# Performance work log

Hardware: AMD Instinct MI355X
Metric: run time of the kernel (lower is better)

The kernel has to match this reference:

```python
import jax, jax.numpy as jnp
import numpy as np

TWO_PI = 2.0 * np.pi
D_IN, N, P, C, BATCH = 784, 1024, 128, 10, 256
T, BETA, K_COUP, A_ANC = 0.5, 2.0, 1.0, 0.08
OMEGA_ANC = TWO_PI * 200.0
N_STEPS = 16  # fixed-grid RK4 steps over [0, T]


def setup_inputs() -> dict:
    key = jax.random.key(0)
    k0, k1, k2, k3 = jax.random.split(key, 4)
    x = jax.random.normal(k0, (BATCH, D_IN), dtype=jnp.float32)
    W_enc = jax.random.normal(k1, (N, D_IN), dtype=jnp.float32) * (1.0 / np.sqrt(D_IN))
    b_enc = jnp.zeros((N,), dtype=jnp.float32)
    xi = jax.random.uniform(k2, (P, N), dtype=jnp.float32) * TWO_PI  # memory patterns
    W_out = jax.random.normal(k3, (C, 2 * N), dtype=jnp.float32) * (1.0 / np.sqrt(2 * N))
    b_out = jnp.zeros((C,), dtype=jnp.float32)
    return {"x": x, "W_enc": W_enc, "b_enc": b_enc, "xi": xi, "W_out": W_out, "b_out": b_out}


def _dphi(t, phi, xi):
    # phi: (B, N), xi: (P, N) -> diff: (B, P, N)
    diff = phi[:, None, :] - xi[None, :, :]
    m = jnp.cos(diff).sum(-1)                               # (B, P) overlaps
    w = jax.nn.softmax(BETA * m / N, axis=-1)               # (B, P)
    coupling = jnp.einsum('bp,bpn->bn', w, jnp.sin(diff))   # (B, N)
    return K_COUP * coupling + A_ANC * jnp.sin(OMEGA_ANC * t - phi)


def reference(x, W_enc, b_enc, xi, W_out, b_out):
    # Encoder: phi0 in (0, 2pi)
    phi0 = TWO_PI * jax.nn.sigmoid(x @ W_enc.T + b_enc)
    dt = T / N_STEPS

    def step(phi, t):
        k1 = _dphi(t, phi, xi)
        k2 = _dphi(t + 0.5 * dt, phi + 0.5 * dt * k1, xi)
        k3 = _dphi(t + 0.5 * dt, phi + 0.5 * dt * k2, xi)
        k4 = _dphi(t + dt, phi + dt * k3, xi)
        return phi + (dt / 6.0) * (k1 + 2.0 * k2 + 2.0 * k3 + k4), None

    ts = jnp.arange(N_STEPS, dtype=jnp.float32) * dt
    phi_T, _ = jax.lax.scan(step, phi0, ts)
    # Readout on [cos, sin] features
    feats = jnp.concatenate([jnp.cos(phi_T), jnp.sin(phi_T)], axis=-1)
    return feats @ W_out.T + b_out
```

## Files before the change

kernel.cpp:

```cpp
#include <hip/hip_runtime.h>
#include <math.h>


typedef __attribute__((ext_vector_type(4))) float f32x4;
typedef __attribute__((ext_vector_type(4))) int   i32x4;
typedef __attribute__((ext_vector_type(8))) short bf16x8;
typedef __attribute__((ext_vector_type(2))) unsigned short u16x2;

struct TCons { float s[64]; float c[64]; };

__device__ __forceinline__ unsigned short f2bf(float f) {
  unsigned u = __builtin_bit_cast(unsigned, f);
  return (unsigned short)((u + 0x7FFFu + ((u >> 16) & 1u)) >> 16);
}
__device__ __forceinline__ int pk4i8(const float* v) {
  int a = __float2int_rn(v[0]*127.0f) & 255;
  int b = __float2int_rn(v[1]*127.0f) & 255;
  int c = __float2int_rn(v[2]*127.0f) & 255;
  int d = __float2int_rn(v[3]*127.0f);
  return a | (b << 8) | (c << 16) | (d << 24);
}

#define A1_OFF    0
#define MBUF_OFF  8192
#define W_OFF     10304
#define ZP_OFF    10560
#define XST_OFF   10576
#define T2L_OFF   13904
#define RED_OFF   13904
#define LDS_BYTES 161360

__global__
__attribute__((amdgpu_flat_work_group_size(1024, 1024), amdgpu_waves_per_eu(4, 4)))
void phasenn_kernel(
    const float* __restrict__ x, const float* __restrict__ W_enc,
    const float* __restrict__ b_enc, const float* __restrict__ xi,
    const float* __restrict__ W_out, const float* __restrict__ b_out,
    float* __restrict__ dout, char* __restrict__ wsb, TCons tc)
{
  __shared__ __align__(16) char smem[LDS_BYTES];

  const int tid  = threadIdx.x;
  const int bk   = blockIdx.x;
  const int w    = tid >> 6;
  const int lane = tid & 63;
  const int q    = lane >> 4;
  const int b16  = lane & 15;
  const int row2 = b16 & 1;
  const int j4   = b16 >> 2;
  const int rp   = (b16 >> 1) & 1;

  char* T1g = wsb;
  char* T2g = wsb + (256 << 10);

  if (tid < 4) *(unsigned*)(smem + ZP_OFF + tid*4) = 0;

  {
    const int row = tid >> 7, dg = tid & 127;
    if (row < 2 && dg < 100) {
      bf16x8 fr = {0,0,0,0,0,0,0,0};
      if (dg < 98) {
        f32x4 v0 = *(const f32x4*)(x + (bk*2 + row)*784 + dg*8);
        f32x4 v1 = *(const f32x4*)(x + (bk*2 + row)*784 + dg*8 + 4);
        #pragma unroll
        for (int i = 0; i < 8; ++i) fr[i] = (short)f2bf(i < 4 ? v0[i] : v1[i-4]);
      }
      *(bf16x8*)(smem + XST_OFF + row*1664 + (((dg ^ row) & 127) << 4)) = fr;
    }
  }

  if (w < 8) {
    const int p = w*16 + b16;
    for (int F = 0; F < 16; ++F) {
      const int n0 = F*64 + q*16;
      f32x4 v0 = *(const f32x4*)(xi + p*1024 + n0);
      f32x4 v1 = *(const f32x4*)(xi + p*1024 + n0 + 4);
      f32x4 v2 = *(const f32x4*)(xi + p*1024 + n0 + 8);
      f32x4 v3 = *(const f32x4*)(xi + p*1024 + n0 + 12);
      float cv[16], sv[16];
      #pragma unroll
      for (int i = 0; i < 16; ++i) {
        float xv = (i < 4) ? v0[i] : (i < 8) ? v1[i-4] : (i < 12) ? v2[i-8] : v3[i-12];
        sv[i] = __sinf(xv); cv[i] = __cosf(xv);
      }
      i32x4 C = { pk4i8(cv), pk4i8(cv+4), pk4i8(cv+8), pk4i8(cv+12) };
      i32x4 S = { pk4i8(sv), pk4i8(sv+4), pk4i8(sv+8), pk4i8(sv+12) };
      char* dst = T1g + (size_t)(w*16 + F)*2048 + lane*16;
      *(i32x4*)(dst) = C; *(i32x4*)(dst + 1024) = S;
    }
  } else {
    const int w2 = w - 8;
    for (int f = 0; f < 16; ++f) {
      const int ct = w2*8 + (f >> 1), P2 = f & 1;
      const int n = ct*16 + b16;
      float cv[16], sv[16];
      #pragma unroll
      for (int i = 0; i < 16; ++i) {
        float xv = xi[(P2*64 + q*16 + i)*1024 + n];
        sv[i] = __sinf(xv); cv[i] = __cosf(xv);
      }
      i32x4 C = { pk4i8(cv), pk4i8(cv+4), pk4i8(cv+8), pk4i8(cv+12) };
      i32x4 S = { pk4i8(sv), pk4i8(sv+4), pk4i8(sv+8), pk4i8(sv+12) };
      char* dst = (ct < 36)
          ? (smem + T2L_OFF + (size_t)(ct*2 + P2)*2048 + lane*16)
          : (T2g + (size_t)(ct*2 + P2)*2048 + lane*16);
      *(i32x4*)(dst) = C; *(i32x4*)(dst + 1024) = S;
    }
  }
  __syncthreads();

  float p0[2], ka[2], pwv[2];
  {
    f32x4 pac[4] = {{0,0,0,0},{0,0,0,0},{0,0,0,0},{0,0,0,0}};
    for (int kt = 0; kt < 25; ++kt) {
      const char* baddr =
          smem + XST_OFF + row2*1664 + ((((kt*4 + q) ^ row2) & 127) << 4);
      bf16x8 bfr = *(const bf16x8*)baddr;
      const int d = kt*32 + q*8;
      #pragma unroll
      for (int j = 0; j < 4; ++j) {
        bf16x8 afr = {0,0,0,0,0,0,0,0};
        if (d < 784) {
          const int n = (w*4 + j)*16 + b16;
          f32x4 v0 = *(const f32x4*)(W_enc + n*784 + d);
          f32x4 v1 = *(const f32x4*)(W_enc + n*784 + d + 4);
          #pragma unroll
          for (int i = 0; i < 8; ++i) afr[i] = (short)f2bf(i < 4 ? v0[i] : v1[i-4]);
        }
        pac[j] = __builtin_amdgcn_mfma_f32_16x16x32_bf16(afr, bfr, pac[j], 0, 0, 0);
      }
    }
    f32x4 pc = (j4==0) ? pac[0] : (j4==1) ? pac[1] : (j4==2) ? pac[2] : pac[3];
    float vA = rp ? pc[2] : pc[0];
    float vB = rp ? pc[3] : pc[1];
    const int n0 = (w*4 + j4)*16 + q*4 + rp*2;
    float ph0 = 6.283185307179586f / (1.0f + __expf(-(vA + b_enc[n0])));
    float ph1 = 6.283185307179586f / (1.0f + __expf(-(vB + b_enc[n0 + 1])));
    p0[0] = ph0; pwv[0] = ph0; ka[0] = 0.0f;
    p0[1] = ph1; pwv[1] = ph1; ka[1] = 0.0f;
  }

  const float dtf = 0.03125f, half = 0.015625f;
  const float sixth = (float)(0.03125/6.0);
  const float mscale = (float)(2.0 / (1024.0 * 16129.0));
  const float kscale = (float)(1.0 / 16129.0);

  for (int e = 0; e < 64; ++e) {
    float csv[2], snv[2];
    {
      #pragma unroll
      for (int r = 0; r < 2; ++r) {
        snv[r] = __sinf(pwv[r]);
        csv[r] = __cosf(pwv[r]);
      }
      int c0 = __float2int_rn(csv[0]*127.0f) & 255;
      int c1 = __float2int_rn(csv[1]*127.0f) & 255;
      int s0 = __float2int_rn(snv[0]*127.0f) & 255;
      int s1 = __float2int_rn(snv[1]*127.0f) & 255;
      const int n0 = (w*4 + j4)*16 + q*4 + rp*2;
      char* base = smem + A1_OFF + row2*2048 + n0;
      *(unsigned short*)(base)        = (unsigned short)(c0 | (c1 << 8));
      *(unsigned short*)(base + 1024) = (unsigned short)(s0 | (s1 << 8));
    }
    __syncthreads();

    {
      const int pt = w & 7, kh = w >> 3;
      i32x4 accC = {0,0,0,0}, accS = {0,0,0,0};
      const char* t1b = T1g + (size_t)(pt*16 + kh*8)*2048 + lane*16;
      const char* a1b = smem + A1_OFF + row2*2048;
      #pragma unroll
      for (int i2 = 0; i2 < 8; ++i2) {
        const int F = kh*8 + i2;
        i32x4 ca = *(const i32x4*)(t1b + (size_t)i2*2048);
        i32x4 sa = *(const i32x4*)(t1b + (size_t)i2*2048 + 1024);
        i32x4 bc = *(const i32x4*)(a1b + F*64 + q*16);
        i32x4 bs = *(const i32x4*)(a1b + 1024 + F*64 + q*16);
        accC = __builtin_amdgcn_mfma_i32_16x16x64_i8(ca, bc, accC, 0, 0, 0);
        accS = __builtin_amdgcn_mfma_i32_16x16x64_i8(sa, bs, accS, 0, 0, 0);
      }
      if (b16 < 2) {
        i32x4 acc = accC + accS;
        *(i32x4*)(smem + MBUF_OFF + kh*1056 + b16*528 + ((pt*16 + q*4) << 2)) = acc;
      }
    }
    __syncthreads();

    if (w < 2) {
      const char* mb = smem + MBUF_OFF + w*528 + lane*8;
      int a0 = *(const int*)(mb),        a1 = *(const int*)(mb + 4);
      int b0 = *(const int*)(mb + 1056), b1 = *(const int*)(mb + 1056 + 4);
      float e0 = __expf((float)(a0 + b0) * mscale);
      float e1 = __expf((float)(a1 + b1) * mscale);
      float s = e0 + e1;
      #pragma unroll
      for (int off = 1; off < 64; off <<= 1) s += __shfl_xor(s, off, 64);
      const float inv = 127.0f / s;
      int w0 = __float2int_rn(e0 * inv);
      int w1 = __float2int_rn(e1 * inv);
      *(unsigned short*)(smem + W_OFF + w*128 + lane*2) =
          (unsigned short)((w0 & 255) | (w1 << 8));
    }
    __syncthreads();

    {
      const float swt = tc.s[e], cwt = tc.c[e];
      const int st = e & 3;
      i32x4 wf0 = *(const i32x4*)(smem + W_OFF + row2*128 + q*16);
      i32x4 wf1 = *(const i32x4*)(smem + W_OFF + row2*128 + 64 + q*16);
      i32x4 aC[4] = {{0,0,0,0},{0,0,0,0},{0,0,0,0},{0,0,0,0}};
      i32x4 aS[4] = {{0,0,0,0},{0,0,0,0},{0,0,0,0},{0,0,0,0}};
      if (w < 9) {
        const char* t2b = smem + T2L_OFF + (size_t)(w*8)*2048 + lane*16;
        #pragma unroll
        for (int c = 0; c < 4; ++c)
          #pragma unroll
          for (int P2 = 0; P2 < 2; ++P2) {
            i32x4 ct_ = *(const i32x4*)(t2b + (size_t)(c*2 + P2)*2048);
            i32x4 st_ = *(const i32x4*)(t2b + (size_t)(c*2 + P2)*2048 + 1024);
            i32x4 wf = P2 ? wf1 : wf0;
            aC[c] = __builtin_amdgcn_mfma_i32_16x16x64_i8(ct_, wf, aC[c], 0, 0, 0);
            aS[c] = __builtin_amdgcn_mfma_i32_16x16x64_i8(st_, wf, aS[c], 0, 0, 0);
          }
      } else {
        const char* t2b = T2g + (size_t)(w*8)*2048 + lane*16;
        #pragma unroll
        for (int c = 0; c < 4; ++c)
          #pragma unroll
          for (int P2 = 0; P2 < 2; ++P2) {
            i32x4 ct_ = *(const i32x4*)(t2b + (size_t)(c*2 + P2)*2048);
            i32x4 st_ = *(const i32x4*)(t2b + (size_t)(c*2 + P2)*2048 + 1024);
            i32x4 wf = P2 ? wf1 : wf0;
            aC[c] = __builtin_amdgcn_mfma_i32_16x16x64_i8(ct_, wf, aC[c], 0, 0, 0);
            aS[c] = __builtin_amdgcn_mfma_i32_16x16x64_i8(st_, wf, aS[c], 0, 0, 0);
          }
      }
      i32x4 c4 = (j4==0) ? aC[0] : (j4==1) ? aC[1] : (j4==2) ? aC[2] : aC[3];
      i32x4 s4 = (j4==0) ? aS[0] : (j4==1) ? aS[1] : (j4==2) ? aS[2] : aS[3];
      float vC[2], vS[2];
      vC[0] = (float)(rp ? c4[2] : c4[0]);  vC[1] = (float)(rp ? c4[3] : c4[1]);
      vS[0] = (float)(rp ? s4[2] : s4[0]);  vS[1] = (float)(rp ? s4[3] : s4[1]);
      #pragma unroll
      for (int r = 0; r < 2; ++r) {
        float s_ = snv[r];
        float c_ = csv[r];
        float kv = (s_*vC[r] - c_*vS[r]) * kscale
                 + 0.08f*(swt*c_ - cwt*s_);
        if (st == 0)      { ka[r]  = kv;           pwv[r] = p0[r] + kv*half; }
        else if (st == 1) { ka[r] += 2.0f*kv;      pwv[r] = p0[r] + kv*half; }
        else if (st == 2) { ka[r] += 2.0f*kv;      pwv[r] = p0[r] + kv*dtf;  }
        else { ka[r] += kv; p0[r] += ka[r]*sixth; pwv[r] = p0[r]; }
      }
    }
  }

  __syncthreads();
  {
    u16x2 cp, sp;
    #pragma unroll
    for (int r = 0; r < 2; ++r) {
      float ph = p0[r];
      cp[r] = f2bf(__cosf(ph)); sp[r] = f2bf(__sinf(ph));
    }
    const int cj = (w*4 + j4)*2 + (q >> 1);
    char* base = smem + A1_OFF + row2*4096 + ((q & 1) << 3) + rp*4;
    *(u16x2*)(base + ((cj ^ row2) << 4))        = cp;
    *(u16x2*)(base + ((cj ^ row2) << 4) + 2048) = sp;
  }
  __syncthreads();
  {
    f32x4 acc = {0.f, 0.f, 0.f, 0.f};
    #pragma unroll
    for (int i2 = 0; i2 < 4; ++i2) {
      const int kt = w*4 + i2;
      const int k = kt*32 + q*8;
      bf16x8 afr = {0,0,0,0,0,0,0,0};
      if (b16 < 10) {
        f32x4 v0 = *(const f32x4*)(W_out + b16*2048 + k);
        f32x4 v1 = *(const f32x4*)(W_out + b16*2048 + k + 4);
        #pragma unroll
        for (int i = 0; i < 8; ++i) afr[i] = (short)f2bf(i < 4 ? v0[i] : v1[i-4]);
      }
      const char* baddr = (b16 < 2)
          ? (smem + A1_OFF + b16*4096 + ((((kt*4 + q) ^ b16) & 255) << 4))
          : (smem + ZP_OFF);
      bf16x8 bfr = *(const bf16x8*)baddr;
      acc = __builtin_amdgcn_mfma_f32_16x16x32_bf16(afr, bfr, acc, 0, 0, 0);
    }
    *(f32x4*)(smem + RED_OFF + ((w*64 + lane) << 4)) = acc;
  }
  __syncthreads();
  if (tid < 64) {
    f32x4 s = {0.f, 0.f, 0.f, 0.f};
    #pragma unroll
    for (int w2 = 0; w2 < 16; ++w2)
      s += *(const f32x4*)(smem + RED_OFF + ((w2*64 + tid) << 4));
    const int b = tid & 15, q2 = tid >> 4;
    if (b < 2) {
      #pragma unroll
      for (int r = 0; r < 4; ++r) {
        const int cl = q2*4 + r;
        if (cl < 10)
          dout[(bk*2 + b)*10 + cl] = s[r] + b_out[cl];
      }
    }
  }
}

extern "C" void kernel_launch(void* const* d_in, const int* in_sizes, int n_in,
                              void* d_out, int out_size, void* d_ws, size_t ws_size,
                              hipStream_t stream) {
  (void)in_sizes; (void)n_in; (void)ws_size; (void)out_size;
  const float* x     = (const float*)d_in[0];
  const float* W_enc = (const float*)d_in[1];
  const float* b_enc = (const float*)d_in[2];
  const float* xi    = (const float*)d_in[3];
  const float* W_out = (const float*)d_in[4];
  const float* b_out = (const float*)d_in[5];
  float* out = (float*)d_out;
  char* wsb = (char*)d_ws;

  TCons tc;
  const double OME = 2.0 * 3.14159265358979323846 * 200.0;
  const double dtd = 0.03125;
  const double co[4] = {0.0, 0.5, 0.5, 1.0};
  for (int e = 0; e < 64; ++e) {
    double t = ((double)(e >> 2) + co[e & 3]) * dtd;
    tc.s[e] = (float)sin(OME * t);
    tc.c[e] = (float)cos(OME * t);
  }

  phasenn_kernel<<<dim3(128), dim3(1024), 0, stream>>>(
      x, W_enc, b_enc, xi, W_out, b_out, out, wsb, tc);
}
```

Measured before the change: 410.3 us.

## Process one sample per block and double grid to fill all CUs

Each block now handles a single batch row instead of two, and the launch grid doubles to 256 blocks. Per-block MFMA work stays about the same because the batch dimension was only padding in 16-wide tiles, so this spreads the work across twice as many compute units. The trade-off is redundant per-block setup and weight-table loads, plus more global/L2 traffic for the shared pattern tables.

Measured after the change: 400.2 us. 1.03x faster.

```diff
diff --git a/kernel.cpp b/kernel.cpp
--- a/kernel.cpp
+++ b/kernel.cpp
@@ -5,7 +5,6 @@
 typedef __attribute__((ext_vector_type(4))) float f32x4;
 typedef __attribute__((ext_vector_type(4))) int   i32x4;
 typedef __attribute__((ext_vector_type(8))) short bf16x8;
-typedef __attribute__((ext_vector_type(2))) unsigned short u16x2;
 
 struct TCons { float s[64]; float c[64]; };
 
@@ -22,13 +21,13 @@
 }
 
 #define A1_OFF    0
-#define MBUF_OFF  8192
-#define W_OFF     10304
-#define ZP_OFF    10560
-#define XST_OFF   10576
-#define T2L_OFF   13904
-#define RED_OFF   13904
-#define LDS_BYTES 161360
+#define MBUF_OFF  4096
+#define W_OFF     5152
+#define ZP_OFF    5408
+#define XST_OFF   5424
+#define T2L_OFF   7104
+#define RED_OFF   7104
+#define LDS_BYTES 154560
 
 __global__
 __attribute__((amdgpu_flat_work_group_size(1024, 1024), amdgpu_waves_per_eu(4, 4)))
@@ -46,27 +45,25 @@
   const int lane = tid & 63;
   const int q    = lane >> 4;
   const int b16  = lane & 15;
-  const int row2 = b16 & 1;
   const int j4   = b16 >> 2;
-  const int rp   = (b16 >> 1) & 1;
+  const int r4   = b16 & 3;
+  const int nph  = (w*4 + j4)*16 + q*4 + r4;
 
   char* T1g = wsb;
   char* T2g = wsb + (256 << 10);
 
   if (tid < 4) *(unsigned*)(smem + ZP_OFF + tid*4) = 0;
 
-  {
-    const int row = tid >> 7, dg = tid & 127;
-    if (row < 2 && dg < 100) {
-      bf16x8 fr = {0,0,0,0,0,0,0,0};
-      if (dg < 98) {
-        f32x4 v0 = *(const f32x4*)(x + (bk*2 + row)*784 + dg*8);
-        f32x4 v1 = *(const f32x4*)(x + (bk*2 + row)*784 + dg*8 + 4);
-        #pragma unroll
-        for (int i = 0; i < 8; ++i) fr[i] = (short)f2bf(i < 4 ? v0[i] : v1[i-4]);
-      }
-      *(bf16x8*)(smem + XST_OFF + row*1664 + (((dg ^ row) & 127) << 4)) = fr;
-    }
+  if (tid < 100) {
+    const int dg = tid;
+    bf16x8 fr = {0,0,0,0,0,0,0,0};
+    if (dg < 98) {
+      f32x4 v0 = *(const f32x4*)(x + (size_t)bk*784 + dg*8);
+      f32x4 v1 = *(const f32x4*)(x + (size_t)bk*784 + dg*8 + 4);
+      #pragma unroll
+      for (int i = 0; i < 8; ++i) fr[i] = (short)f2bf(i < 4 ? v0[i] : v1[i-4]);
+    }
+    *(bf16x8*)(smem + XST_OFF + (dg << 4)) = fr;
   }
 
   if (w < 8) {
@@ -109,13 +106,11 @@
   }
   __syncthreads();
 
-  float p0[2], ka[2], pwv[2];
+  float p0, ka, pwv;
   {
     f32x4 pac[4] = {{0,0,0,0},{0,0,0,0},{0,0,0,0},{0,0,0,0}};
     for (int kt = 0; kt < 25; ++kt) {
-      const char* baddr =
-          smem + XST_OFF + row2*1664 + ((((kt*4 + q) ^ row2) & 127) << 4);
-      bf16x8 bfr = *(const bf16x8*)baddr;
+      bf16x8 bfr = *(const bf16x8*)(smem + XST_OFF + ((kt*4 + q) << 4));
       const int d = kt*32 + q*8;
       #pragma unroll
       for (int j = 0; j < 4; ++j) {
@@ -131,13 +126,9 @@
       }
     }
     f32x4 pc = (j4==0) ? pac[0] : (j4==1) ? pac[1] : (j4==2) ? pac[2] : pac[3];
-    float vA = rp ? pc[2] : pc[0];
-    float vB = rp ? pc[3] : pc[1];
-    const int n0 = (w*4 + j4)*16 + q*4 + rp*2;
-    float ph0 = 6.283185307179586f / (1.0f + __expf(-(vA + b_enc[n0])));
-    float ph1 = 6.283185307179586f / (1.0f + __expf(-(vB + b_enc[n0 + 1])));
-    p0[0] = ph0; pwv[0] = ph0; ka[0] = 0.0f;
-    p0[1] = ph1; pwv[1] = ph1; ka[1] = 0.0f;
+    float vA = (r4==0) ? pc[0] : (r4==1) ? pc[1] : (r4==2) ? pc[2] : pc[3];
+    float ph = 6.283185307179586f / (1.0f + __expf(-(vA + b_enc[nph])));
+    p0 = ph; pwv = ph; ka = 0.0f;
   }
 
   const float dtf = 0.03125f, half = 0.015625f;
@@ -145,22 +136,15 @@
   const float mscale = (float)(2.0 / (1024.0 * 16129.0));
   const float kscale = (float)(1.0 / 16129.0);
 
+  char* a1wr = smem + A1_OFF + nph;
+
   for (int e = 0; e < 64; ++e) {
-    float csv[2], snv[2];
+    float csv, snv;
     {
-      #pragma unroll
-      for (int r = 0; r < 2; ++r) {
-        snv[r] = __sinf(pwv[r]);
-        csv[r] = __cosf(pwv[r]);
-      }
-      int c0 = __float2int_rn(csv[0]*127.0f) & 255;
-      int c1 = __float2int_rn(csv[1]*127.0f) & 255;
-      int s0 = __float2int_rn(snv[0]*127.0f) & 255;
-      int s1 = __float2int_rn(snv[1]*127.0f) & 255;
-      const int n0 = (w*4 + j4)*16 + q*4 + rp*2;
-      char* base = smem + A1_OFF + row2*2048 + n0;
-      *(unsigned short*)(base)        = (unsigned short)(c0 | (c1 << 8));
-      *(unsigned short*)(base + 1024) = (unsigned short)(s0 | (s1 << 8));
+      snv = __sinf(pwv);
+      csv = __cosf(pwv);
+      *(char*)(a1wr)        = (char)(__float2int_rn(csv*127.0f));
+      *(char*)(a1wr + 1024) = (char)(__float2int_rn(snv*127.0f));
     }
     __syncthreads();
 
@@ -168,28 +152,27 @@
       const int pt = w & 7, kh = w >> 3;
       i32x4 accC = {0,0,0,0}, accS = {0,0,0,0};
       const char* t1b = T1g + (size_t)(pt*16 + kh*8)*2048 + lane*16;
-      const char* a1b = smem + A1_OFF + row2*2048;
+      const char* a1b = smem + A1_OFF + kh*512 + q*16;
       #pragma unroll
       for (int i2 = 0; i2 < 8; ++i2) {
-        const int F = kh*8 + i2;
         i32x4 ca = *(const i32x4*)(t1b + (size_t)i2*2048);
         i32x4 sa = *(const i32x4*)(t1b + (size_t)i2*2048 + 1024);
-        i32x4 bc = *(const i32x4*)(a1b + F*64 + q*16);
-        i32x4 bs = *(const i32x4*)(a1b + 1024 + F*64 + q*16);
+        i32x4 bc = *(const i32x4*)(a1b + i2*64);
+        i32x4 bs = *(const i32x4*)(a1b + i2*64 + 1024);
         accC = __builtin_amdgcn_mfma_i32_16x16x64_i8(ca, bc, accC, 0, 0, 0);
         accS = __builtin_amdgcn_mfma_i32_16x16x64_i8(sa, bs, accS, 0, 0, 0);
       }
-      if (b16 < 2) {
+      if (b16 == 0) {
         i32x4 acc = accC + accS;
-        *(i32x4*)(smem + MBUF_OFF + kh*1056 + b16*528 + ((pt*16 + q*4) << 2)) = acc;
+        *(i32x4*)(smem + MBUF_OFF + kh*528 + ((pt*16 + q*4) << 2)) = acc;
       }
     }
     __syncthreads();
 
-    if (w < 2) {
-      const char* mb = smem + MBUF_OFF + w*528 + lane*8;
-      int a0 = *(const int*)(mb),        a1 = *(const int*)(mb + 4);
-      int b0 = *(const int*)(mb + 1056), b1 = *(const int*)(mb + 1056 + 4);
+    if (w == 0) {
+      const char* mb = smem + MBUF_OFF + lane*8;
+      int a0 = *(const int*)(mb),       a1 = *(const int*)(mb + 4);
+      int b0 = *(const int*)(mb + 528), b1 = *(const int*)(mb + 528 + 4);
       float e0 = __expf((float)(a0 + b0) * mscale);
       float e1 = __expf((float)(a1 + b1) * mscale);
       float s = e0 + e1;
@@ -198,7 +181,7 @@
       const float inv = 127.0f / s;
       int w0 = __float2int_rn(e0 * inv);
       int w1 = __float2int_rn(e1 * inv);
-      *(unsigned short*)(smem + W_OFF + w*128 + lane*2) =
+      *(unsigned short*)(smem + W_OFF + lane*2) =
           (unsigned short)((w0 & 255) | (w1 << 8));
     }
     __syncthreads();
@@ -206,8 +189,8 @@
     {
       const float swt = tc.s[e], cwt = tc.c[e];
       const int st = e & 3;
-      i32x4 wf0 = *(const i32x4*)(smem + W_OFF + row2*128 + q*16);
-      i32x4 wf1 = *(const i32x4*)(smem + W_OFF + row2*128 + 64 + q*16);
+      i32x4 wf0 = *(const i32x4*)(smem + W_OFF + q*16);
+      i32x4 wf1 = *(const i32x4*)(smem + W_OFF + 64 + q*16);
       i32x4 aC[4] = {{0,0,0,0},{0,0,0,0},{0,0,0,0},{0,0,0,0}};
       i32x4 aS[4] = {{0,0,0,0},{0,0,0,0},{0,0,0,0},{0,0,0,0}};
       if (w < 9) {
@@ -237,35 +220,21 @@
       }
       i32x4 c4 = (j4==0) ? aC[0] : (j4==1) ? aC[1] : (j4==2) ? aC[2] : aC[3];
       i32x4 s4 = (j4==0) ? aS[0] : (j4==1) ? aS[1] : (j4==2) ? aS[2] : aS[3];
-      float vC[2], vS[2];
-      vC[0] = (float)(rp ? c4[2] : c4[0]);  vC[1] = (float)(rp ? c4[3] : c4[1]);
-      vS[0] = (float)(rp ? s4[2] : s4[0]);  vS[1] = (float)(rp ? s4[3] : s4[1]);
-      #pragma unroll
-      for (int r = 0; r < 2; ++r) {
-        float s_ = snv[r];
-        float c_ = csv[r];
-        float kv = (s_*vC[r] - c_*vS[r]) * kscale
-                 + 0.08f*(swt*c_ - cwt*s_);
-        if (st == 0)      { ka[r]  = kv;           pwv[r] = p0[r] + kv*half; }
-        else if (st == 1) { ka[r] += 2.0f*kv;      pwv[r] = p0[r] + kv*half; }
-        else if (st == 2) { ka[r] += 2.0f*kv;      pwv[r] = p0[r] + kv*dtf;  }
-        else { ka[r] += kv; p0[r] += ka[r]*sixth; pwv[r] = p0[r]; }
-      }
+      float vC = (float)((r4==0) ? c4[0] : (r4==1) ? c4[1] : (r4==2) ? c4[2] : c4[3]);
+      float vS = (float)((r4==0) ? s4[0] : (r4==1) ? s4[1] : (r4==2) ? s4[2] : s4[3]);
+      float kv = (snv*vC - csv*vS) * kscale
+               + 0.08f*(swt*csv - cwt*snv);
+      if (st == 0)      { ka  = kv;           pwv = p0 + kv*half; }
+      else if (st == 1) { ka += 2.0f*kv;      pwv = p0 + kv*half; }
+      else if (st == 2) { ka += 2.0f*kv;      pwv = p0 + kv*dtf;  }
+      else { ka += kv; p0 += ka*sixth; pwv = p0; }
     }
   }
 
   __syncthreads();
   {
-    u16x2 cp, sp;
-    #pragma unroll
-    for (int r = 0; r < 2; ++r) {
-      float ph = p0[r];
-      cp[r] = f2bf(__cosf(ph)); sp[r] = f2bf(__sinf(ph));
-    }
-    const int cj = (w*4 + j4)*2 + (q >> 1);
-    char* base = smem + A1_OFF + row2*4096 + ((q & 1) << 3) + rp*4;
-    *(u16x2*)(base + ((cj ^ row2) << 4))        = cp;
-    *(u16x2*)(base + ((cj ^ row2) << 4) + 2048) = sp;
+    *(unsigned short*)(smem + A1_OFF + nph*2)        = f2bf(__cosf(p0));
+    *(unsigned short*)(smem + A1_OFF + 2048 + nph*2) = f2bf(__sinf(p0));
   }
   __syncthreads();
   {
@@ -281,8 +250,8 @@
         #pragma unroll
         for (int i = 0; i < 8; ++i) afr[i] = (short)f2bf(i < 4 ? v0[i] : v1[i-4]);
       }
-      const char* baddr = (b16 < 2)
-          ? (smem + A1_OFF + b16*4096 + ((((kt*4 + q) ^ b16) & 255) << 4))
+      const char* baddr = (b16 == 0)
+          ? (smem + A1_OFF + ((kt*4 + q) << 4))
           : (smem + ZP_OFF);
       bf16x8 bfr = *(const bf16x8*)baddr;
       acc = __builtin_amdgcn_mfma_f32_16x16x32_bf16(afr, bfr, acc, 0, 0, 0);
@@ -296,12 +265,12 @@
     for (int w2 = 0; w2 < 16; ++w2)
       s += *(const f32x4*)(smem + RED_OFF + ((w2*64 + tid) << 4));
     const int b = tid & 15, q2 = tid >> 4;
-    if (b < 2) {
+    if (b == 0) {
       #pragma unroll
       for (int r = 0; r < 4; ++r) {
         const int cl = q2*4 + r;
         if (cl < 10)
-          dout[(bk*2 + b)*10 + cl] = s[r] + b_out[cl];
+          dout[(size_t)bk*10 + cl] = s[r] + b_out[cl];
       }
     }
   }
@@ -330,6 +299,6 @@
     tc.c[e] = (float)cos(OME * t);
   }
 
-  phasenn_kernel<<<dim3(128), dim3(1024), 0, stream>>>(
+  phasenn_kernel<<<dim3(256), dim3(1024), 0, stream>>>(
       x, W_enc, b_enc, xi, W_out, b_out, out, wsb, tc);
 }
```
